# Kernel tuning notes

Hardware: AMD Instinct MI355X
Metric: run time of the kernel (lower is better)

The kernel has to match this reference:

```python
import jax, jax.numpy as jnp
import numpy as np

N_NODES = 8192
IN_DIM = 20000
HID = 256
LAT = 64
N_EDGES = 262144


def setup_inputs() -> dict:
    key = jax.random.key(0)
    ks = jax.random.split(key, 12)
    s_in = 1.0 / np.sqrt(IN_DIM)
    s_h = 1.0 / np.sqrt(HID)
    s_l = 1.0 / np.sqrt(LAT)
    return {
        "x": jax.random.normal(ks[0], (N_NODES, IN_DIM), jnp.float32),
        "edge_index": jax.random.randint(ks[1], (2, N_EDGES), 0, N_NODES, jnp.int64 if jax.config.jax_enable_x64 else jnp.int32),
        "w_gcn": jax.random.uniform(ks[2], (IN_DIM, HID), jnp.float32, -s_in, s_in),
        "b_gcn": jnp.zeros((HID,), jnp.float32),
        "w_enc": jax.random.uniform(ks[3], (HID, LAT), jnp.float32, -s_h, s_h),
        "b_enc": jax.random.uniform(ks[4], (LAT,), jnp.float32, -s_h, s_h),
        "w_d1": jax.random.uniform(ks[5], (LAT, HID), jnp.float32, -s_l, s_l),
        "b_d1": jax.random.uniform(ks[6], (HID,), jnp.float32, -s_l, s_l),
        "w_d2": jax.random.uniform(ks[7], (HID, IN_DIM), jnp.float32, -s_h, s_h),
        "b_d2": jax.random.uniform(ks[8], (IN_DIM,), jnp.float32, -s_h, s_h),
    }


def _gcn_conv(x, edge_index, w, b):
    """PyG GCNConv (add_self_loops=True, normalize=True): A_hat @ (x W) + b."""
    n = x.shape[0]
    h = x @ w  # [N, HID] -- project first (in_dim >> out_dim)
    loops = jnp.arange(n, dtype=edge_index.dtype)
    row = jnp.concatenate([edge_index[0], loops])  # source nodes
    col = jnp.concatenate([edge_index[1], loops])  # target nodes
    deg = jax.ops.segment_sum(jnp.ones_like(col, dtype=h.dtype), col, num_segments=n)
    dinv = jnp.where(deg > 0, jax.lax.rsqrt(deg), 0.0)
    norm = dinv[row] * dinv[col]  # [E+N]
    msg = h[row] * norm[:, None]  # gather + scale
    out = jax.ops.segment_sum(msg, col, num_segments=n)  # scatter-add
    return out + b


def reference(x, edge_index, w_gcn, b_gcn, w_enc, b_enc, w_d1, b_d1, w_d2, b_d2):
    # Encoder: GCNConv -> ReLU -> (Dropout: eval no-op) -> Linear
    h = _gcn_conv(x, edge_index, w_gcn, b_gcn)
    latent = jax.nn.relu(h) @ w_enc + b_enc  # [N, LAT]
    # Decoder: Linear -> ReLU -> (Dropout) -> Linear
    recon = jax.nn.relu(latent @ w_d1 + b_d1) @ w_d2 + b_d2  # [N, IN_DIM]
    return recon, latent
```

## Files before the change

kernel.cpp:

```cpp
#include <hip/hip_runtime.h>
#include <stdint.h>

typedef short short8 __attribute__((ext_vector_type(8)));
typedef float f32x4 __attribute__((ext_vector_type(4)));

#define N_NODES 8192
#define IN_DIM 20000
#define HIDDEN 256
#define LATENT 64
#define N_EDGES 262144
#define K_STEPS 625
#define RECON_ELEMS (8192LL * 20000LL)
#define WD2T_ROWS 20096
#define NSUB3 313

static __device__ __forceinline__ unsigned short f2bf(float f) {
  union { float f; unsigned int u; } v;
  v.f = f;
  unsigned int u = v.u;
  return (unsigned short)((u + 0x7FFFu + ((u >> 16) & 1u)) >> 16);
}

__global__ void k_count(const int* __restrict__ col, int* __restrict__ cnt) {
  int e = blockIdx.x * 256 + threadIdx.x;
  if (e < N_EDGES) atomicAdd(&cnt[col[e]], 1);
}

__global__ void k_dinv(const int* __restrict__ cnt, float* __restrict__ dinv) {
  int i = blockIdx.x * 256 + threadIdx.x;
  if (i < N_NODES) dinv[i] = rsqrtf((float)(cnt[i] + 1));
}

__global__ void k_scan(const int* __restrict__ cnt, int* __restrict__ offs,
                       int* __restrict__ cursor) {
  __shared__ int ps[256];
  int t = threadIdx.x;
  int local[32];
  int s = 0;
#pragma unroll
  for (int i = 0; i < 32; ++i) { local[i] = cnt[t * 32 + i]; s += local[i]; }
  ps[t] = s;
  __syncthreads();
  for (int d = 1; d < 256; d <<= 1) {
    int v = (t >= d) ? ps[t - d] : 0;
    __syncthreads();
    ps[t] += v;
    __syncthreads();
  }
  int pre = (t == 0) ? 0 : ps[t - 1];
#pragma unroll
  for (int i = 0; i < 32; ++i) {
    offs[t * 32 + i] = pre;
    cursor[t * 32 + i] = pre;
    pre += local[i];
  }
  if (t == 255) offs[N_NODES] = pre;
}

__global__ void k_fill(const int* __restrict__ row, const int* __restrict__ col,
                       int* __restrict__ cursor, int* __restrict__ csr_src) {
  int e = blockIdx.x * 256 + threadIdx.x;
  if (e < N_EDGES) {
    int c = col[e];
    int pos = atomicAdd(&cursor[c], 1);
    csr_src[pos] = row[e];
  }
}

__global__ void k_pack_wgcn(const float* __restrict__ w, unsigned short* __restrict__ pk) {
  int s = blockIdx.x;
  int t = threadIdx.x;
  int k0 = s * 32;
  unsigned int packed[16];
#pragma unroll
  for (int j = 0; j < 16; ++j) {
    float a = w[(size_t)(k0 + 2 * j) * HIDDEN + t];
    float b = w[(size_t)(k0 + 2 * j + 1) * HIDDEN + t];
    packed[j] = (unsigned)f2bf(a) | ((unsigned)f2bf(b) << 16);
  }
  int sw = (t >> 1) & 3;
  uint4* dst = (uint4*)(pk + ((size_t)s * HIDDEN + t) * 32);
#pragma unroll
  for (int j = 0; j < 4; ++j)
    dst[j ^ sw] = make_uint4(packed[4 * j], packed[4 * j + 1], packed[4 * j + 2], packed[4 * j + 3]);
}

__global__ void k_twd2(const float* __restrict__ wd2, unsigned short* __restrict__ wd2t) {
  __shared__ float tile[HIDDEN * 64];
  int n0 = blockIdx.x * 64;
  int t = threadIdx.x;
  int tk = t >> 6;
  int tn = t & 63;
#pragma unroll 4
  for (int kb = 0; kb < 64; ++kb) {
    int k = kb * 4 + tk;
    int n = n0 + tn;
    tile[k * 64 + tn] = (n < IN_DIM) ? wd2[(size_t)k * IN_DIM + n] : 0.0f;
  }
  __syncthreads();
  int rl = t >> 2;
  int q = t & 3;
  unsigned int packed[32];
#pragma unroll
  for (int j = 0; j < 32; ++j) {
    float a = tile[(q * 64 + 2 * j) * 64 + rl];
    float b = tile[(q * 64 + 2 * j + 1) * 64 + rl];
    packed[j] = (unsigned)f2bf(a) | ((unsigned)f2bf(b) << 16);
  }
  int rs = rl & 7;
  uint4* dst = (uint4*)(wd2t + (size_t)(n0 + rl) * HIDDEN + q * 64);
#pragma unroll
  for (int j = 0; j < 8; ++j)
    dst[j ^ rs] = make_uint4(packed[4 * j], packed[4 * j + 1], packed[4 * j + 2], packed[4 * j + 3]);
}

__global__ __launch_bounds__(512, 4)
void k_gemm1(const float* __restrict__ x, const unsigned short* __restrict__ wpk,
             float* __restrict__ h0p) {
  const int m0 = blockIdx.x * 64;
  const int split = blockIdx.y;
  const int s_beg = (K_STEPS * split) >> 2;
  const int s_end = (K_STEPS * (split + 1)) >> 2;

  const int t = threadIdx.x;
  const int lane = t & 63;
  const int wid = t >> 6;
  const int wm = wid >> 2;
  const int wn = wid & 3;
  const int lr = lane & 15;
  const int lg = lane >> 4;

  __shared__ unsigned short Alds[2][64 * 40];
  __shared__ unsigned short Blds[2][256 * 32];

  const int arow = t >> 3;
  const int ak = (t & 7) * 4;
  const float* xrow = x + (size_t)(m0 + arow) * IN_DIM + ak;

  f32x4 acc[2][4];
#pragma unroll
  for (int i = 0; i < 2; ++i)
#pragma unroll
    for (int j = 0; j < 4; ++j) acc[i][j] = (f32x4){0.f, 0.f, 0.f, 0.f};

  auto stageB = [&](int s, int buf) {
    const unsigned short* g = wpk + (size_t)s * (HIDDEN * 32) + wid * 512 + lane * 8;
    __builtin_amdgcn_global_load_lds(
        (const __attribute__((address_space(1))) unsigned int*)g,
        (__attribute__((address_space(3))) unsigned int*)&Blds[buf][wid * 512], 16, 0, 0);
    __builtin_amdgcn_global_load_lds(
        (const __attribute__((address_space(1))) unsigned int*)(g + 4096),
        (__attribute__((address_space(3))) unsigned int*)&Blds[buf][4096 + wid * 512], 16, 0, 0);
  };

  float4 areg = *(const float4*)(xrow + (size_t)s_beg * 32);
  stageB(s_beg, 0);
  {
    uint2 ap;
    ap.x = (unsigned)f2bf(areg.x) | ((unsigned)f2bf(areg.y) << 16);
    ap.y = (unsigned)f2bf(areg.z) | ((unsigned)f2bf(areg.w) << 16);
    *(uint2*)&Alds[0][arow * 40 + ak] = ap;
  }
  __syncthreads();

  int cur = 0;
  for (int s = s_beg; s < s_end; ++s) {
    const bool more = (s + 1 < s_end);
    if (more) {
      areg = *(const float4*)(xrow + (size_t)(s + 1) * 32);
      stageB(s + 1, cur ^ 1);
    }
    {
      short8 a0 = *(const short8*)&Alds[cur][(wm * 32 + lr) * 40 + lg * 8];
      short8 a1 = *(const short8*)&Alds[cur][(wm * 32 + 16 + lr) * 40 + lg * 8];
#pragma unroll
      for (int nt = 0; nt < 4; ++nt) {
        int n = wn * 64 + nt * 16 + lr;
        short8 b = *(const short8*)&Blds[cur][n * 32 + ((lg ^ ((n >> 1) & 3)) * 8)];
        acc[0][nt] = __builtin_amdgcn_mfma_f32_16x16x32_bf16(a0, b, acc[0][nt], 0, 0, 0);
        acc[1][nt] = __builtin_amdgcn_mfma_f32_16x16x32_bf16(a1, b, acc[1][nt], 0, 0, 0);
      }
    }
    __syncthreads();
    if (more) {
      uint2 ap;
      ap.x = (unsigned)f2bf(areg.x) | ((unsigned)f2bf(areg.y) << 16);
      ap.y = (unsigned)f2bf(areg.z) | ((unsigned)f2bf(areg.w) << 16);
      *(uint2*)&Alds[cur ^ 1][arow * 40 + ak] = ap;
      __syncthreads();
    }
    cur ^= 1;
  }

  float* outp = h0p + (size_t)split * (N_NODES * HIDDEN) + (size_t)m0 * HIDDEN;
#pragma unroll
  for (int mt = 0; mt < 2; ++mt)
#pragma unroll
    for (int nt = 0; nt < 4; ++nt) {
      int col = wn * 64 + nt * 16 + lr;
#pragma unroll
      for (int r = 0; r < 4; ++r) {
        int rowi = wm * 32 + mt * 16 + lg * 4 + r;
        outp[rowi * HIDDEN + col] = acc[mt][nt][r];
      }
    }
}

__global__ void k_sum(const float* __restrict__ p, float* __restrict__ h0) {
  int i = blockIdx.x * 256 + threadIdx.x;
  float4 a = ((const float4*)p)[i];
  float4 b = ((const float4*)p)[i + (N_NODES * HIDDEN / 4)];
  float4 c = ((const float4*)p)[i + 2 * (N_NODES * HIDDEN / 4)];
  float4 d = ((const float4*)p)[i + 3 * (N_NODES * HIDDEN / 4)];
  float4 r;
  r.x = (a.x + b.x) + (c.x + d.x);
  r.y = (a.y + b.y) + (c.y + d.y);
  r.z = (a.z + b.z) + (c.z + d.z);
  r.w = (a.w + b.w) + (c.w + d.w);
  ((float4*)h0)[i] = r;
}

__global__ void k_agg(const float* __restrict__ h0, const float* __restrict__ dinv,
                      const int* __restrict__ offs, const int* __restrict__ csr_src,
                      const float* __restrict__ bias, float* __restrict__ hrelu) {
  int c = blockIdx.x;
  int t = threadIdx.x;
  float dc = dinv[c];
  float acc = h0[(size_t)c * HIDDEN + t] * dc * dc;
  int beg = offs[c], end = offs[c + 1];
  for (int i = beg; i < end; ++i) {
    int r = csr_src[i];
    float wgt = dinv[r] * dc;
    acc += h0[(size_t)r * HIDDEN + t] * wgt;
  }
  float v = acc + bias[t];
  hrelu[(size_t)c * HIDDEN + t] = v > 0.f ? v : 0.f;
}

__global__ void k_enc(const float* __restrict__ hrelu, const float* __restrict__ w_enc,
                      const float* __restrict__ b_enc, float* __restrict__ latent) {
  __shared__ float hrow[4 * HIDDEN];
  int nb = blockIdx.x * 4;
  int t = threadIdx.x;
#pragma unroll
  for (int j = 0; j < 4; ++j) hrow[j * HIDDEN + t] = hrelu[(size_t)(nb + j) * HIDDEN + t];
  __syncthreads();
  int lat = t & 63;
  int nl = t >> 6;
  float acc = b_enc[lat];
#pragma unroll 8
  for (int k = 0; k < HIDDEN; ++k)
    acc += hrow[nl * HIDDEN + k] * w_enc[k * LATENT + lat];
  latent[(size_t)(nb + nl) * LATENT + lat] = acc;
}

__global__ void k_dec1(const float* __restrict__ latent, const float* __restrict__ w_d1,
                       const float* __restrict__ b_d1, unsigned short* __restrict__ hid2) {
  __shared__ float lrow[4 * LATENT];
  int nb = blockIdx.x * 4;
  int t = threadIdx.x;
  lrow[t] = latent[(size_t)nb * LATENT + t];
  __syncthreads();
  float b = b_d1[t];
  float a0 = b, a1 = b, a2 = b, a3 = b;
#pragma unroll 8
  for (int k = 0; k < LATENT; ++k) {
    float wv = w_d1[k * HIDDEN + t];
    a0 += lrow[k] * wv;
    a1 += lrow[LATENT + k] * wv;
    a2 += lrow[2 * LATENT + k] * wv;
    a3 += lrow[3 * LATENT + k] * wv;
  }
  hid2[(size_t)nb * HIDDEN + t]       = f2bf(a0 > 0.f ? a0 : 0.f);
  hid2[(size_t)(nb + 1) * HIDDEN + t] = f2bf(a1 > 0.f ? a1 : 0.f);
  hid2[(size_t)(nb + 2) * HIDDEN + t] = f2bf(a2 > 0.f ? a2 : 0.f);
  hid2[(size_t)(nb + 3) * HIDDEN + t] = f2bf(a3 > 0.f ? a3 : 0.f);
}

__global__ __launch_bounds__(256, 2)
void k_gemm3(const unsigned short* __restrict__ hid2, const unsigned short* __restrict__ wd2t,
             const float* __restrict__ b_d2, float* __restrict__ recon) {
  __shared__ unsigned short Bl[2][64 * 256];
  __shared__ float TB[4 * 512];
  const int t = threadIdx.x;
  const int lane = t & 63;
  const int wid = t >> 6;
  const int wm = wid >> 1;
  const int wn = wid & 1;
  const int lr = lane & 15;
  const int lg = lane >> 4;
  const int m0 = blockIdx.x * 128;
  const int chunk = blockIdx.y;
  const int s0 = (NSUB3 * chunk) >> 3;
  const int s1 = (NSUB3 * (chunk + 1)) >> 3;

  short8 a[4][8];
#pragma unroll
  for (int mt = 0; mt < 4; ++mt)
#pragma unroll
    for (int ks = 0; ks < 8; ++ks)
      a[mt][ks] = *(const short8*)(hid2 + (size_t)(m0 + wm * 64 + mt * 16 + lr) * 256 + ks * 32 + lg * 8);

  auto stage = [&](int sub, int buf) {
#pragma unroll
    for (int i = 0; i < 8; ++i) {
      const unsigned short* g = wd2t + (size_t)sub * (64 * 256) + ((wid * 8 + i) * 512 + lane * 8);
      unsigned short* l = &Bl[buf][(wid * 8 + i) * 512];
      __builtin_amdgcn_global_load_lds(
          (const __attribute__((address_space(1))) unsigned int*)g,
          (__attribute__((address_space(3))) unsigned int*)l, 16, 0, 0);
    }
  };

  stage(s0, 0);
  __syncthreads();

  int cur = 0;
  for (int sub = s0; sub < s1; ++sub) {
    if (sub + 1 < s1) stage(sub + 1, cur ^ 1);

    f32x4 acc[4][2];
#pragma unroll
    for (int i = 0; i < 4; ++i) {
      acc[i][0] = (f32x4){0.f, 0.f, 0.f, 0.f};
      acc[i][1] = (f32x4){0.f, 0.f, 0.f, 0.f};
    }

    const int rl0 = wn * 32 + lr;
    const int rl1 = rl0 + 16;
#pragma unroll
    for (int ks = 0; ks < 8; ++ks) {
      short8 b0 = *(const short8*)&Bl[cur][rl0 * 256 + (((ks * 4 + lg) ^ (rl0 & 7)) << 3)];
      short8 b1 = *(const short8*)&Bl[cur][rl1 * 256 + (((ks * 4 + lg) ^ (rl1 & 7)) << 3)];
#pragma unroll
      for (int mt = 0; mt < 4; ++mt) {
        acc[mt][0] = __builtin_amdgcn_mfma_f32_16x16x32_bf16(a[mt][ks], b0, acc[mt][0], 0, 0, 0);
        acc[mt][1] = __builtin_amdgcn_mfma_f32_16x16x32_bf16(a[mt][ks], b1, acc[mt][1], 0, 0, 0);
      }
    }

    const int cg = (lane & 7) * 4;
    const int gc = sub * 64 + wn * 32 + cg;
    f32x4 bias4 = (f32x4){0.f, 0.f, 0.f, 0.f};
    if (gc < IN_DIM) bias4 = *(const f32x4*)&b_d2[gc];
    float* TBw = TB + wid * 512;
#pragma unroll
    for (int mt = 0; mt < 4; ++mt) {
#pragma unroll
      for (int nt = 0; nt < 2; ++nt)
#pragma unroll
        for (int r = 0; r < 4; ++r) {
          int row = lg * 4 + r;
          TBw[row * 32 + ((nt * 16 + lr) ^ (((row >> 2) & 1) << 4))] = acc[mt][nt][r];
        }
#pragma unroll
      for (int p = 0; p < 2; ++p) {
        int row = p * 8 + (lane >> 3);
        f32x4 v = *(const f32x4*)&TBw[row * 32 + (cg ^ (((row >> 2) & 1) << 4))];
        if (gc < IN_DIM) {
          int gr = m0 + wm * 64 + mt * 16 + row;
          *(f32x4*)&recon[(size_t)gr * IN_DIM + gc] = v + bias4;
        }
      }
    }
    __syncthreads();
    cur ^= 1;
  }
}

extern "C" void kernel_launch(void* const* d_in, const int* in_sizes, int n_in,
                              void* d_out, int out_size, void* d_ws, size_t ws_size,
                              hipStream_t stream) {
  const float* x     = (const float*)d_in[0];
  const int*   edge  = (const int*)d_in[1];
  const float* w_gcn = (const float*)d_in[2];
  const float* b_gcn = (const float*)d_in[3];
  const float* w_enc = (const float*)d_in[4];
  const float* b_enc = (const float*)d_in[5];
  const float* w_d1  = (const float*)d_in[6];
  const float* b_d1  = (const float*)d_in[7];
  const float* w_d2  = (const float*)d_in[8];
  const float* b_d2  = (const float*)d_in[9];
  float* out = (float*)d_out;
  (void)in_sizes; (void)n_in; (void)out_size; (void)ws_size;

  char* ws = (char*)d_ws;
  size_t o = 0;
  auto alloc = [&](size_t bytes) {
    char* p = ws + o;
    o += (bytes + 255) & ~(size_t)255;
    return p;
  };
  unsigned short* wpk  = (unsigned short*)alloc((size_t)K_STEPS * HIDDEN * 32 * 2);
  unsigned short* wd2t = (unsigned short*)alloc((size_t)WD2T_ROWS * HIDDEN * 2);
  float* h0p  = (float*)alloc((size_t)4 * N_NODES * HIDDEN * 4);
  float* h0   = (float*)alloc((size_t)N_NODES * HIDDEN * 4);
  float* hrel = (float*)alloc((size_t)N_NODES * HIDDEN * 4);
  unsigned short* hid2 = (unsigned short*)alloc((size_t)N_NODES * HIDDEN * 2);
  int* cnt    = (int*)alloc(N_NODES * 4);
  float* dinv = (float*)alloc(N_NODES * 4);
  int* offs   = (int*)alloc((N_NODES + 1) * 4);
  int* cursor = (int*)alloc(N_NODES * 4);
  int* csr    = (int*)alloc((size_t)N_EDGES * 4);

  const int* erow = edge;
  const int* ecol = edge + N_EDGES;

  hipMemsetAsync(cnt, 0, N_NODES * 4, stream);
  k_count<<<N_EDGES / 256, 256, 0, stream>>>(ecol, cnt);
  k_scan<<<1, 256, 0, stream>>>(cnt, offs, cursor);
  k_dinv<<<N_NODES / 256, 256, 0, stream>>>(cnt, dinv);
  k_fill<<<N_EDGES / 256, 256, 0, stream>>>(erow, ecol, cursor, csr);
  k_pack_wgcn<<<K_STEPS, 256, 0, stream>>>(w_gcn, wpk);
  k_twd2<<<WD2T_ROWS / 64, 256, 0, stream>>>(w_d2, wd2t);
  k_gemm1<<<dim3(N_NODES / 64, 4), 512, 0, stream>>>(x, wpk, h0p);
  k_sum<<<(N_NODES * HIDDEN / 4) / 256, 256, 0, stream>>>(h0p, h0);
  k_agg<<<N_NODES, 256, 0, stream>>>(h0, dinv, offs, csr, b_gcn, hrel);
  float* latent = out + RECON_ELEMS;
  k_enc<<<N_NODES / 4, 256, 0, stream>>>(hrel, w_enc, b_enc, latent);
  k_dec1<<<N_NODES / 4, 256, 0, stream>>>(latent, w_d1, b_d1, hid2);
  k_gemm3<<<dim3(N_NODES / 128, 8), 256, 0, stream>>>(hid2, wd2t, b_d2, out);
}
```

Measured before the change: 630.1 us.

## Shrink GEMM tiles and load activation fragments directly to registers

In the first GEMM, the activation tile no longer goes through shared memory. Each lane loads its x fragment straight from global memory, converts it to bf16 in registers, and feeds the MFMA, which removes an LDS round trip and one barrier per step. The M tile is halved to 32 rows with 256 threads, giving more blocks. The decoder GEMM tile is halved to 32 columns per sub-step with 16 chunks and higher occupancy. The trade-off is less reuse of W per block and more redundant global reads of x across the four wave columns.

```diff
diff --git a/kernel.cpp b/kernel.cpp
--- a/kernel.cpp
+++ b/kernel.cpp
@@ -12,13 +12,17 @@
 #define K_STEPS 625
 #define RECON_ELEMS (8192LL * 20000LL)
 #define WD2T_ROWS 20096
-#define NSUB3 313
+#define NSUB3 626
 
 static __device__ __forceinline__ unsigned short f2bf(float f) {
   union { float f; unsigned int u; } v;
   v.f = f;
   unsigned int u = v.u;
   return (unsigned short)((u + 0x7FFFu + ((u >> 16) & 1u)) >> 16);
+}
+
+static __device__ __forceinline__ unsigned pk2bf(float a, float b) {
+  return (unsigned)f2bf(a) | ((unsigned)f2bf(b) << 16);
 }
 
 __global__ void k_count(const int* __restrict__ col, int* __restrict__ cnt) {
@@ -76,7 +80,7 @@
   for (int j = 0; j < 16; ++j) {
     float a = w[(size_t)(k0 + 2 * j) * HIDDEN + t];
     float b = w[(size_t)(k0 + 2 * j + 1) * HIDDEN + t];
-    packed[j] = (unsigned)f2bf(a) | ((unsigned)f2bf(b) << 16);
+    packed[j] = pk2bf(a, b);
   }
   int sw = (t >> 1) & 3;
   uint4* dst = (uint4*)(pk + ((size_t)s * HIDDEN + t) * 32);
@@ -105,7 +109,7 @@
   for (int j = 0; j < 32; ++j) {
     float a = tile[(q * 64 + 2 * j) * 64 + rl];
     float b = tile[(q * 64 + 2 * j + 1) * 64 + rl];
-    packed[j] = (unsigned)f2bf(a) | ((unsigned)f2bf(b) << 16);
+    packed[j] = pk2bf(a, b);
   }
   int rs = rl & 7;
   uint4* dst = (uint4*)(wd2t + (size_t)(n0 + rl) * HIDDEN + q * 64);
@@ -114,28 +118,24 @@
     dst[j ^ rs] = make_uint4(packed[4 * j], packed[4 * j + 1], packed[4 * j + 2], packed[4 * j + 3]);
 }
 
-__global__ __launch_bounds__(512, 4)
+__global__ __launch_bounds__(256, 4)
 void k_gemm1(const float* __restrict__ x, const unsigned short* __restrict__ wpk,
              float* __restrict__ h0p) {
-  const int m0 = blockIdx.x * 64;
+  const int m0 = blockIdx.x * 32;
   const int split = blockIdx.y;
   const int s_beg = (K_STEPS * split) >> 2;
   const int s_end = (K_STEPS * (split + 1)) >> 2;
 
   const int t = threadIdx.x;
   const int lane = t & 63;
-  const int wid = t >> 6;
-  const int wm = wid >> 2;
-  const int wn = wid & 3;
+  const int wn = t >> 6;
   const int lr = lane & 15;
   const int lg = lane >> 4;
 
-  __shared__ unsigned short Alds[2][64 * 40];
   __shared__ unsigned short Blds[2][256 * 32];
 
-  const int arow = t >> 3;
-  const int ak = (t & 7) * 4;
-  const float* xrow = x + (size_t)(m0 + arow) * IN_DIM + ak;
+  const float* arow0 = x + (size_t)(m0 + lr) * IN_DIM + lg * 8;
+  const float* arow1 = x + (size_t)(m0 + 16 + lr) * IN_DIM + lg * 8;
 
   f32x4 acc[2][4];
 #pragma unroll
@@ -144,51 +144,46 @@
     for (int j = 0; j < 4; ++j) acc[i][j] = (f32x4){0.f, 0.f, 0.f, 0.f};
 
   auto stageB = [&](int s, int buf) {
-    const unsigned short* g = wpk + (size_t)s * (HIDDEN * 32) + wid * 512 + lane * 8;
-    __builtin_amdgcn_global_load_lds(
-        (const __attribute__((address_space(1))) unsigned int*)g,
-        (__attribute__((address_space(3))) unsigned int*)&Blds[buf][wid * 512], 16, 0, 0);
-    __builtin_amdgcn_global_load_lds(
-        (const __attribute__((address_space(1))) unsigned int*)(g + 4096),
-        (__attribute__((address_space(3))) unsigned int*)&Blds[buf][4096 + wid * 512], 16, 0, 0);
+#pragma unroll
+    for (int i = 0; i < 4; ++i) {
+      const unsigned short* g = wpk + (size_t)s * (HIDDEN * 32) + (wn * 4 + i) * 512 + lane * 8;
+      __builtin_amdgcn_global_load_lds(
+          (const __attribute__((address_space(1))) unsigned int*)g,
+          (__attribute__((address_space(3))) unsigned int*)&Blds[buf][(wn * 4 + i) * 512], 16, 0, 0);
+    }
   };
 
-  float4 areg = *(const float4*)(xrow + (size_t)s_beg * 32);
+  float4 u0 = *(const float4*)(arow0 + (size_t)s_beg * 32);
+  float4 u1 = *(const float4*)(arow0 + (size_t)s_beg * 32 + 4);
+  float4 u2 = *(const float4*)(arow1 + (size_t)s_beg * 32);
+  float4 u3 = *(const float4*)(arow1 + (size_t)s_beg * 32 + 4);
   stageB(s_beg, 0);
-  {
-    uint2 ap;
-    ap.x = (unsigned)f2bf(areg.x) | ((unsigned)f2bf(areg.y) << 16);
-    ap.y = (unsigned)f2bf(areg.z) | ((unsigned)f2bf(areg.w) << 16);
-    *(uint2*)&Alds[0][arow * 40 + ak] = ap;
-  }
   __syncthreads();
 
   int cur = 0;
   for (int s = s_beg; s < s_end; ++s) {
     const bool more = (s + 1 < s_end);
+    float4 v0, v1, v2, v3;
     if (more) {
-      areg = *(const float4*)(xrow + (size_t)(s + 1) * 32);
       stageB(s + 1, cur ^ 1);
-    }
-    {
-      short8 a0 = *(const short8*)&Alds[cur][(wm * 32 + lr) * 40 + lg * 8];
-      short8 a1 = *(const short8*)&Alds[cur][(wm * 32 + 16 + lr) * 40 + lg * 8];
-#pragma unroll
-      for (int nt = 0; nt < 4; ++nt) {
-        int n = wn * 64 + nt * 16 + lr;
-        short8 b = *(const short8*)&Blds[cur][n * 32 + ((lg ^ ((n >> 1) & 3)) * 8)];
-        acc[0][nt] = __builtin_amdgcn_mfma_f32_16x16x32_bf16(a0, b, acc[0][nt], 0, 0, 0);
-        acc[1][nt] = __builtin_amdgcn_mfma_f32_16x16x32_bf16(a1, b, acc[1][nt], 0, 0, 0);
-      }
+      v0 = *(const float4*)(arow0 + (size_t)(s + 1) * 32);
+      v1 = *(const float4*)(arow0 + (size_t)(s + 1) * 32 + 4);
+      v2 = *(const float4*)(arow1 + (size_t)(s + 1) * 32);
+      v3 = *(const float4*)(arow1 + (size_t)(s + 1) * 32 + 4);
+    }
+    uint4 af0 = make_uint4(pk2bf(u0.x, u0.y), pk2bf(u0.z, u0.w), pk2bf(u1.x, u1.y), pk2bf(u1.z, u1.w));
+    uint4 af1 = make_uint4(pk2bf(u2.x, u2.y), pk2bf(u2.z, u2.w), pk2bf(u3.x, u3.y), pk2bf(u3.z, u3.w));
+    short8 a0 = *(short8*)&af0;
+    short8 a1 = *(short8*)&af1;
+#pragma unroll
+    for (int nt = 0; nt < 4; ++nt) {
+      int n = wn * 64 + nt * 16 + lr;
+      short8 b = *(const short8*)&Blds[cur][n * 32 + ((lg ^ ((n >> 1) & 3)) * 8)];
+      acc[0][nt] = __builtin_amdgcn_mfma_f32_16x16x32_bf16(a0, b, acc[0][nt], 0, 0, 0);
+      acc[1][nt] = __builtin_amdgcn_mfma_f32_16x16x32_bf16(a1, b, acc[1][nt], 0, 0, 0);
     }
     __syncthreads();
-    if (more) {
-      uint2 ap;
-      ap.x = (unsigned)f2bf(areg.x) | ((unsigned)f2bf(areg.y) << 16);
-      ap.y = (unsigned)f2bf(areg.z) | ((unsigned)f2bf(areg.w) << 16);
-      *(uint2*)&Alds[cur ^ 1][arow * 40 + ak] = ap;
-      __syncthreads();
-    }
+    u0 = v0; u1 = v1; u2 = v2; u3 = v3;
     cur ^= 1;
   }
 
@@ -200,7 +195,7 @@
       int col = wn * 64 + nt * 16 + lr;
 #pragma unroll
       for (int r = 0; r < 4; ++r) {
-        int rowi = wm * 32 + mt * 16 + lg * 4 + r;
+        int rowi = mt * 16 + lg * 4 + r;
         outp[rowi * HIDDEN + col] = acc[mt][nt][r];
       }
     }
@@ -277,35 +272,34 @@
   hid2[(size_t)(nb + 3) * HIDDEN + t] = f2bf(a3 > 0.f ? a3 : 0.f);
 }
 
-__global__ __launch_bounds__(256, 2)
+__global__ __launch_bounds__(256, 4)
 void k_gemm3(const unsigned short* __restrict__ hid2, const unsigned short* __restrict__ wd2t,
              const float* __restrict__ b_d2, float* __restrict__ recon) {
-  __shared__ unsigned short Bl[2][64 * 256];
+  __shared__ unsigned short Bl[2][32 * 256];
   __shared__ float TB[4 * 512];
   const int t = threadIdx.x;
   const int lane = t & 63;
   const int wid = t >> 6;
-  const int wm = wid >> 1;
-  const int wn = wid & 1;
+  const int wm = wid;
   const int lr = lane & 15;
   const int lg = lane >> 4;
   const int m0 = blockIdx.x * 128;
   const int chunk = blockIdx.y;
-  const int s0 = (NSUB3 * chunk) >> 3;
-  const int s1 = (NSUB3 * (chunk + 1)) >> 3;
-
-  short8 a[4][8];
-#pragma unroll
-  for (int mt = 0; mt < 4; ++mt)
+  const int s0 = (NSUB3 * chunk) >> 4;
+  const int s1 = (NSUB3 * (chunk + 1)) >> 4;
+
+  short8 a[2][8];
+#pragma unroll
+  for (int mt = 0; mt < 2; ++mt)
 #pragma unroll
     for (int ks = 0; ks < 8; ++ks)
-      a[mt][ks] = *(const short8*)(hid2 + (size_t)(m0 + wm * 64 + mt * 16 + lr) * 256 + ks * 32 + lg * 8);
+      a[mt][ks] = *(const short8*)(hid2 + (size_t)(m0 + wm * 32 + mt * 16 + lr) * 256 + ks * 32 + lg * 8);
 
   auto stage = [&](int sub, int buf) {
 #pragma unroll
-    for (int i = 0; i < 8; ++i) {
-      const unsigned short* g = wd2t + (size_t)sub * (64 * 256) + ((wid * 8 + i) * 512 + lane * 8);
-      unsigned short* l = &Bl[buf][(wid * 8 + i) * 512];
+    for (int i = 0; i < 4; ++i) {
+      const unsigned short* g = wd2t + (size_t)sub * (32 * 256) + ((wid * 4 + i) * 512 + lane * 8);
+      unsigned short* l = &Bl[buf][(wid * 4 + i) * 512];
       __builtin_amdgcn_global_load_lds(
           (const __attribute__((address_space(1))) unsigned int*)g,
           (__attribute__((address_space(3))) unsigned int*)l, 16, 0, 0);
@@ -319,33 +313,33 @@
   for (int sub = s0; sub < s1; ++sub) {
     if (sub + 1 < s1) stage(sub + 1, cur ^ 1);
 
-    f32x4 acc[4][2];
-#pragma unroll
-    for (int i = 0; i < 4; ++i) {
+    f32x4 acc[2][2];
+#pragma unroll
+    for (int i = 0; i < 2; ++i) {
       acc[i][0] = (f32x4){0.f, 0.f, 0.f, 0.f};
       acc[i][1] = (f32x4){0.f, 0.f, 0.f, 0.f};
     }
 
-    const int rl0 = wn * 32 + lr;
-    const int rl1 = rl0 + 16;
+    const int rl0 = lr;
+    const int rl1 = 16 + lr;
 #pragma unroll
     for (int ks = 0; ks < 8; ++ks) {
       short8 b0 = *(const short8*)&Bl[cur][rl0 * 256 + (((ks * 4 + lg) ^ (rl0 & 7)) << 3)];
       short8 b1 = *(const short8*)&Bl[cur][rl1 * 256 + (((ks * 4 + lg) ^ (rl1 & 7)) << 3)];
 #pragma unroll
-      for (int mt = 0; mt < 4; ++mt) {
+      for (int mt = 0; mt < 2; ++mt) {
         acc[mt][0] = __builtin_amdgcn_mfma_f32_16x16x32_bf16(a[mt][ks], b0, acc[mt][0], 0, 0, 0);
         acc[mt][1] = __builtin_amdgcn_mfma_f32_16x16x32_bf16(a[mt][ks], b1, acc[mt][1], 0, 0, 0);
       }
     }
 
     const int cg = (lane & 7) * 4;
-    const int gc = sub * 64 + wn * 32 + cg;
+    const int gc = sub * 32 + cg;
     f32x4 bias4 = (f32x4){0.f, 0.f, 0.f, 0.f};
     if (gc < IN_DIM) bias4 = *(const f32x4*)&b_d2[gc];
     float* TBw = TB + wid * 512;
 #pragma unroll
-    for (int mt = 0; mt < 4; ++mt) {
+    for (int mt = 0; mt < 2; ++mt) {
 #pragma unroll
       for (int nt = 0; nt < 2; ++nt)
 #pragma unroll
@@ -358,7 +352,7 @@
         int row = p * 8 + (lane >> 3);
         f32x4 v = *(const f32x4*)&TBw[row * 32 + (cg ^ (((row >> 2) & 1) << 4))];
         if (gc < IN_DIM) {
-          int gr = m0 + wm * 64 + mt * 16 + row;
+          int gr = m0 + wm * 32 + mt * 16 + row;
           *(f32x4*)&recon[(size_t)gr * IN_DIM + gc] = v + bias4;
         }
       }
@@ -413,11 +407,11 @@
   k_fill<<<N_EDGES / 256, 256, 0, stream>>>(erow, ecol, cursor, csr);
   k_pack_wgcn<<<K_STEPS, 256, 0, stream>>>(w_gcn, wpk);
   k_twd2<<<WD2T_ROWS / 64, 256, 0, stream>>>(w_d2, wd2t);
-  k_gemm1<<<dim3(N_NODES / 64, 4), 512, 0, stream>>>(x, wpk, h0p);
+  k_gemm1<<<dim3(N_NODES / 32, 4), 256, 0, stream>>>(x, wpk, h0p);
   k_sum<<<(N_NODES * HIDDEN / 4) / 256, 256, 0, stream>>>(h0p, h0);
   k_agg<<<N_NODES, 256, 0, stream>>>(h0, dinv, offs, csr, b_gcn, hrel);
   float* latent = out + RECON_ELEMS;
   k_enc<<<N_NODES / 4, 256, 0, stream>>>(hrel, w_enc, b_enc, latent);
   k_dec1<<<N_NODES / 4, 256, 0, stream>>>(latent, w_d1, b_d1, hid2);
-  k_gemm3<<<dim3(N_NODES / 128, 8), 256, 0, stream>>>(hid2, wd2t, b_d2, out);
-}
+  k_gemm3<<<dim3(N_NODES / 128, 16), 256, 0, stream>>>(hid2, wd2t, b_d2, out);
+}
```

New measurement: 817.6 us. 29.8% more time.
